# Optimization experiments

Measured on AMD Instinct MI355X. Metric: run time of the kernel, lower is better.

Reference implementation:

```python
import jax, jax.numpy as jnp
import numpy as np

E = 512      # embed_dim
H = 8        # num_heads
HD = E // H  # head_dim
TGT = 512
SRC = 2048
B = 16


def setup_inputs() -> dict:
    key = jax.random.key(0)
    ks = jax.random.split(key, 10)
    inp = {
        "query": jax.random.normal(ks[0], (TGT, B, E), dtype=jnp.float32),
        "key": jax.random.normal(ks[1], (SRC, B, E), dtype=jnp.float32),
        "value": jax.random.normal(ks[2], (SRC, B, E), dtype=jnp.float32),
        "in_proj_weight": jax.random.normal(ks[3], (3 * E, E), dtype=jnp.float32) * 0.02,
        "in_proj_bias": jax.random.normal(ks[4], (3 * E,), dtype=jnp.float32) * 0.02,
        "bias_k": jax.random.normal(ks[5], (1, 1, E), dtype=jnp.float32) * 0.02,
        "bias_v": jax.random.normal(ks[6], (1, 1, E), dtype=jnp.float32) * 0.02,
        "out_proj_weight": jax.random.normal(ks[7], (E, E), dtype=jnp.float32) * 0.02,
        "out_proj_bias": jnp.zeros((E,), dtype=jnp.float32),
        "key_padding_mask": jax.random.randint(ks[8], (B, SRC), 0, 2).astype(bool),
    }
    return inp


def reference(query, key, value, in_proj_weight, in_proj_bias, bias_k, bias_v,
              out_proj_weight, out_proj_bias, key_padding_mask):
    tgt_len, bsz, embed_dim = query.shape
    scaling = float(HD) ** -0.5

    # manual in-projection (query != key, key is value -> separate q, fused kv)
    q = query @ in_proj_weight[:E].T + in_proj_bias[:E]
    k = key @ in_proj_weight[E:2 * E].T + in_proj_bias[E:2 * E]
    v = value @ in_proj_weight[2 * E:].T + in_proj_bias[2 * E:]
    q = q * scaling

    # bias_k / bias_v concatenation along src dim; pad key_padding_mask with False
    k = jnp.concatenate([k, jnp.broadcast_to(bias_k, (1, bsz, E))], axis=0)
    v = jnp.concatenate([v, jnp.broadcast_to(bias_v, (1, bsz, E))], axis=0)
    kpm = jnp.pad(key_padding_mask, ((0, 0), (0, 1)))  # [B, SRC+1]

    src_len = k.shape[0]
    # [len, B, E] -> [B*H, len, HD]
    q = q.reshape(tgt_len, bsz * H, HD).transpose(1, 0, 2)
    k = k.reshape(src_len, bsz * H, HD).transpose(1, 0, 2)
    v = v.reshape(src_len, bsz * H, HD).transpose(1, 0, 2)

    scores = jnp.einsum('bth,bsh->bts', q, k)  # [B*H, TGT, SRC+1]
    mask = kpm[:, None, None, :]               # [B, 1, 1, SRC+1]
    scores = scores.reshape(bsz, H, tgt_len, src_len)
    scores = jnp.where(mask, -jnp.inf, scores).reshape(bsz * H, tgt_len, src_len)
    attn = jax.nn.softmax(scores, axis=-1)

    out = jnp.einsum('bts,bsh->bth', attn, v)                 # [B*H, TGT, HD]
    out = out.transpose(1, 0, 2).reshape(tgt_len, bsz, E)     # [TGT, B, E]
    out = out @ out_proj_weight.T + out_proj_bias
    return out, attn
```

## Files before the change

kernel.cpp:

```cpp
#include <hip/hip_runtime.h>
#include <hip/hip_bf16.h>

#define E    512
#define H    8
#define HD   64
#define TGT  512
#define SRC  2048
#define S1   2049
#define S1P  2112
#define NB   16
#define BH   128
#define NCH  33
#define PW   2120

typedef __attribute__((ext_vector_type(8))) short short8;
typedef __attribute__((ext_vector_type(4))) float floatx4;

__device__ __forceinline__ unsigned short f2bf(float x) {
    unsigned u = __float_as_uint(x);
    u = (u + 0x7FFF + ((u >> 16) & 1)) >> 16;
    return (unsigned short)u;
}

__device__ __forceinline__ int4 cvt8(const float4 f0, const float4 f1) {
    __hip_bfloat162 o[4];
    o[0] = __float22bfloat162_rn({f0.x, f0.y});
    o[1] = __float22bfloat162_rn({f0.z, f0.w});
    o[2] = __float22bfloat162_rn({f1.x, f1.y});
    o[3] = __float22bfloat162_rn({f1.z, f1.w});
    return *(int4*)o;
}

__global__ __launch_bounds__(256) void proj_gemm(const float* __restrict__ X,
    const float* __restrict__ W, const float* __restrict__ bias,
    unsigned short* __restrict__ Y, const int ld, const float scale)
{
    __shared__ __align__(16) unsigned short As[128][72];
    __shared__ __align__(16) unsigned short Bs[64][72];
    const int tid  = threadIdx.x;
    const int c0   = blockIdx.x << 6;
    const int r0   = blockIdx.y << 7;
    const int w    = tid >> 6, lane = tid & 63, c = lane & 15, quad = lane >> 4;
    floatx4 acc[2][4] = {};
    for (int k0 = 0; k0 < E; k0 += 64) {
#pragma unroll
        for (int i = 0; i < 4; ++i) {
            const int idx = tid + (i << 8);
            const int r = idx >> 3, q = (idx & 7) << 3;
            const float4 f0 = *(const float4*)&X[(size_t)(r0 + r) * E + k0 + q];
            const float4 f1 = *(const float4*)&X[(size_t)(r0 + r) * E + k0 + q + 4];
            *(int4*)&As[r][q] = cvt8(f0, f1);
        }
#pragma unroll
        for (int i = 0; i < 2; ++i) {
            const int idx = tid + (i << 8);
            const int r = idx >> 3, q = (idx & 7) << 3;
            const float4 f0 = *(const float4*)&W[(size_t)(c0 + r) * E + k0 + q];
            const float4 f1 = *(const float4*)&W[(size_t)(c0 + r) * E + k0 + q + 4];
            *(int4*)&Bs[r][q] = cvt8(f0, f1);
        }
        __syncthreads();
#pragma unroll
        for (int kh = 0; kh < 2; ++kh) {
            short8 a0 = *(const short8*)&As[(w << 5) + c][(kh << 5) + (quad << 3)];
            short8 a1 = *(const short8*)&As[(w << 5) + 16 + c][(kh << 5) + (quad << 3)];
#pragma unroll
            for (int n = 0; n < 4; ++n) {
                short8 b = *(const short8*)&Bs[(n << 4) + c][(kh << 5) + (quad << 3)];
                acc[0][n] = __builtin_amdgcn_mfma_f32_16x16x32_bf16(a0, b, acc[0][n], 0, 0, 0);
                acc[1][n] = __builtin_amdgcn_mfma_f32_16x16x32_bf16(a1, b, acc[1][n], 0, 0, 0);
            }
        }
        __syncthreads();
    }
#pragma unroll
    for (int mt = 0; mt < 2; ++mt) {
#pragma unroll
        for (int reg = 0; reg < 4; ++reg) {
            const int rg = r0 + (w << 5) + (mt << 4) + (quad << 2) + reg;
            const int t = rg >> 4, b = rg & 15;
#pragma unroll
            for (int n = 0; n < 4; ++n) {
                const int col = c0 + (n << 4) + c;
                const int h = col >> 6, hd = col & 63;
                const float v = (acc[mt][n][reg] + bias[col]) * scale;
                Y[((size_t)(b * H + h) * ld + t) * HD + hd] = f2bf(v);
            }
        }
    }
}

#define FB_BIAS  8192
#define FB_KPAD  64512
#define FB_VPAD  516096
__global__ __launch_bounds__(256) void fill_bias(const float* __restrict__ bk,
    const float* __restrict__ bv,
    unsigned short* __restrict__ kbuf, unsigned short* __restrict__ vtbuf)
{
    const int idx = blockIdx.x * 256 + threadIdx.x;
    if (idx < FB_BIAS) {
        const int bh = idx >> 6, hd = idx & 63, h = bh & 7;
        kbuf[((size_t)bh * S1P + SRC) * HD + hd] = f2bf(bk[h * HD + hd]);
        vtbuf[((size_t)bh * HD + hd) * S1P + SRC] = f2bf(bv[h * HD + hd]);
    } else if (idx < FB_BIAS + FB_KPAD) {
        const int i = idx - FB_BIAS;
        const int bh = i / 504, o = i % 504;
        const int4 z = {0, 0, 0, 0};
        ((int4*)&kbuf[((size_t)bh * S1P + S1) * HD])[o] = z;
    } else if (idx < FB_BIAS + FB_KPAD + FB_VPAD) {
        const int i = idx - FB_BIAS - FB_KPAD;
        const int bh = i / 4032, r = i % 4032;
        const int hd = r / 63, s = S1 + r % 63;
        vtbuf[((size_t)bh * HD + hd) * S1P + s] = 0;
    }
}

__global__ __launch_bounds__(256) void transpose_v(const unsigned short* __restrict__ vbuf,
    unsigned short* __restrict__ vtbuf)
{
    __shared__ __align__(16) unsigned short T[64][72];
    const int tid = threadIdx.x;
    const int s0  = blockIdx.x << 6;
    const int bh  = blockIdx.y;
#pragma unroll
    for (int i = 0; i < 2; ++i) {
        const int idx = tid + (i << 8);
        const int s = idx >> 3, q = (idx & 7) << 3;
        *(int4*)&T[s][q] = *(const int4*)&vbuf[((size_t)bh * SRC + s0 + s) * HD + q];
    }
    __syncthreads();
#pragma unroll
    for (int i = 0; i < 2; ++i) {
        const int idx = tid + (i << 8);
        const int hd = idx >> 3, sq = (idx & 7) << 3;
        unsigned short tmp[8];
#pragma unroll
        for (int j = 0; j < 8; ++j) tmp[j] = T[sq + j][hd];
        *(int4*)&vtbuf[((size_t)bh * HD + hd) * S1P + s0 + sq] = *(int4*)tmp;
    }
}

__global__ __launch_bounds__(512, 4) void attn_fused(
    const unsigned short* __restrict__ qbh,
    const unsigned short* __restrict__ kbuf,
    const unsigned short* __restrict__ vtbuf,
    const int* __restrict__ kpm,
    float* __restrict__ attn, unsigned short* __restrict__ ctx)
{
    __shared__ __align__(16) unsigned short P[16][PW];
    __shared__ float cpart[16][68];
    __shared__ float sums[8][16];
    __shared__ float linv[16];
    const int tid  = threadIdx.x;
    const int orig = blockIdx.y * 32 + blockIdx.x;
    const int swz  = (orig & 7) * 512 + (orig >> 3);
    const int t0   = (swz & 31) << 4;
    const int bh   = swz >> 5;
    const int bb   = bh >> 3;
    const int w = tid >> 6, lane = tid & 63, c = lane & 15, quad = lane >> 4;

    const unsigned short* qr = &qbh[((size_t)bh * TGT + t0 + c) * HD + (quad << 3)];
    short8 qa0 = *(const short8*)qr;
    short8 qa1 = *(const short8*)(qr + 32);

#define LOADK(D0, D1, M, CH) do {                                               \
        const unsigned short* kb_ = &kbuf[((size_t)bh * S1P + ((CH) << 6)) * HD]; \
        _Pragma("unroll")                                                       \
        for (int n_ = 0; n_ < 4; ++n_) {                                        \
            const unsigned short* kr_ = kb_ + ((n_ << 4) + c) * HD + (quad << 3); \
            D0[n_] = *(const short8*)kr_;                                       \
            D1[n_] = *(const short8*)(kr_ + 32);                                \
        }                                                                       \
        _Pragma("unroll")                                                       \
        for (int n_ = 0; n_ < 4; ++n_) {                                        \
            const int s_ = ((CH) << 6) + (n_ << 4) + c;                         \
            M[n_] = (s_ < SRC) ? (kpm[bb * SRC + s_] ? 3e38f : 0.f)             \
                               : ((s_ == SRC) ? 0.f : 3e38f);                   \
        }                                                                       \
    } while (0)

#define QK_COMPUTE(CH, B0, B1, M) do {                                          \
        const int s0_ = (CH) << 6;                                              \
        floatx4 sc_[4] = {};                                                    \
        _Pragma("unroll")                                                       \
        for (int n_ = 0; n_ < 4; ++n_) {                                        \
            sc_[n_] = __builtin_amdgcn_mfma_f32_16x16x32_bf16(qa0, B0[n_], sc_[n_], 0, 0, 0); \
            sc_[n_] = __builtin_amdgcn_mfma_f32_16x16x32_bf16(qa1, B1[n_], sc_[n_], 0, 0, 0); \
        }                                                                       \
        _Pragma("unroll")                                                       \
        for (int n_ = 0; n_ < 4; ++n_) {                                        \
            _Pragma("unroll")                                                   \
            for (int rg_ = 0; rg_ < 4; ++rg_) {                                 \
                const float p_ = __expf(sc_[n_][rg_] - M[n_]);                  \
                rs[rg_] += p_;                                                  \
                P[(quad << 2) + rg_][s0_ + (n_ << 4) + c] = f2bf(p_);           \
            }                                                                   \
        }                                                                       \
    } while (0)

    float rs[4] = {0.f, 0.f, 0.f, 0.f};
    short8 kb0[4], kb1[4];
    float mk[4];
    LOADK(kb0, kb1, mk, w);
    int ch;
    for (ch = w; ch + 8 < NCH; ch += 8) {
        short8 nb0[4], nb1[4];
        float nm[4];
        LOADK(nb0, nb1, nm, ch + 8);
        QK_COMPUTE(ch, kb0, kb1, mk);
#pragma unroll
        for (int n = 0; n < 4; ++n) { kb0[n] = nb0[n]; kb1[n] = nb1[n]; mk[n] = nm[n]; }
    }
    QK_COMPUTE(ch, kb0, kb1, mk);

#pragma unroll
    for (int reg = 0; reg < 4; ++reg) {
        float v = rs[reg];
        v += __shfl_xor(v, 1); v += __shfl_xor(v, 2);
        v += __shfl_xor(v, 4); v += __shfl_xor(v, 8);
        rs[reg] = v;
    }
    if (c == 0) {
#pragma unroll
        for (int reg = 0; reg < 4; ++reg)
            sums[w][(quad << 2) + reg] = rs[reg];
    }
    __syncthreads();
    if (tid < 16) {
        float s = 0.f;
#pragma unroll
        for (int i = 0; i < 8; ++i) s += sums[i][tid];
        linv[tid] = 1.0f / s;
    }
    __syncthreads();

    const int hs = w & 3, kh2 = w >> 2;
    const int base = kh2 * 1056;
    const unsigned short* vrow = &vtbuf[((size_t)bh * HD + (hs << 4) + c) * S1P + base];
#define LV(U) (*(const short8*)&vrow[((U) << 5) + (quad << 3)])
#define LP(U) (*(const short8*)&P[c][base + ((U) << 5) + (quad << 3)])
    floatx4 ca0 = {}, ca1 = {};
    short8 vt = LV(32);
    short8 v0 = LV(0), v1 = LV(1), v2 = LV(2), v3 = LV(3);
#pragma unroll
    for (int u = 0; u < 32; u += 4) {
        ca0 = __builtin_amdgcn_mfma_f32_16x16x32_bf16(LP(u),     v0, ca0, 0, 0, 0);
        ca1 = __builtin_amdgcn_mfma_f32_16x16x32_bf16(LP(u + 1), v1, ca1, 0, 0, 0);
        if (u < 28) { v0 = LV(u + 4); v1 = LV(u + 5); }
        ca0 = __builtin_amdgcn_mfma_f32_16x16x32_bf16(LP(u + 2), v2, ca0, 0, 0, 0);
        ca1 = __builtin_amdgcn_mfma_f32_16x16x32_bf16(LP(u + 3), v3, ca1, 0, 0, 0);
        if (u < 28) { v2 = LV(u + 6); v3 = LV(u + 7); }
    }
    ca0 = __builtin_amdgcn_mfma_f32_16x16x32_bf16(LP(32), vt, ca0, 0, 0, 0);
    if (kh2 == 1) {
#pragma unroll
        for (int reg = 0; reg < 4; ++reg)
            cpart[(quad << 2) + reg][(hs << 4) + c] = ca0[reg] + ca1[reg];
    }
    __syncthreads();
    if (kh2 == 0) {
#pragma unroll
        for (int reg = 0; reg < 4; ++reg) {
            const int row = (quad << 2) + reg;
            const float v = (ca0[reg] + ca1[reg] + cpart[row][(hs << 4) + c]) * linv[row];
            ctx[((size_t)bh * TGT + t0 + row) * HD + (hs << 4) + c] = f2bf(v);
        }
    }

    for (int p = w; p < 16; p += 8) {
        const int s0 = p << 7;
#pragma unroll
        for (int r = 0; r < 16; ++r) {
            const unsigned pk = *(const unsigned*)&P[r][s0 + (lane << 1)];
            const float li = linv[r];
            const size_t a = ((size_t)bh * TGT + t0 + r) * S1 + s0 + (lane << 1);
            attn[a]     = __uint_as_float((pk & 0xFFFFu) << 16) * li;
            attn[a + 1] = __uint_as_float(pk & 0xFFFF0000u) * li;
        }
    }
    if (w == 7 && lane < 16) {
        const float p = __uint_as_float((unsigned)P[lane][2048] << 16) * linv[lane];
        attn[((size_t)bh * TGT + t0 + lane) * S1 + 2048] = p;
    }
#undef LOADK
#undef QK_COMPUTE
#undef LV
#undef LP
}

__global__ __launch_bounds__(256) void outproj_gemm(const unsigned short* __restrict__ ctx,
    const float* __restrict__ W, const float* __restrict__ bias,
    float* __restrict__ out)
{
    __shared__ __align__(16) unsigned short As[128][72];
    __shared__ __align__(16) unsigned short Bs[64][72];
    const int tid = threadIdx.x;
    const int c0  = blockIdx.x << 6;
    const int r0  = blockIdx.y << 7;
    const int w   = tid >> 6, lane = tid & 63, c = lane & 15, quad = lane >> 4;
    floatx4 acc[2][4] = {};
    for (int k0 = 0; k0 < E; k0 += 64) {
        const int h = k0 >> 6;
#pragma unroll
        for (int i = 0; i < 4; ++i) {
            const int idx = tid + (i << 8);
            const int r = idx >> 3, q = (idx & 7) << 3;
            const int rg = r0 + r, t = rg >> 4, b = rg & 15;
            *(int4*)&As[r][q] = *(const int4*)&ctx[((size_t)(b * H + h) * TGT + t) * HD + q];
        }
#pragma unroll
        for (int i = 0; i < 2; ++i) {
            const int idx = tid + (i << 8);
            const int r = idx >> 3, q = (idx & 7) << 3;
            const float4 f0 = *(const float4*)&W[(size_t)(c0 + r) * E + k0 + q];
            const float4 f1 = *(const float4*)&W[(size_t)(c0 + r) * E + k0 + q + 4];
            *(int4*)&Bs[r][q] = cvt8(f0, f1);
        }
        __syncthreads();
#pragma unroll
        for (int kh = 0; kh < 2; ++kh) {
            short8 a0 = *(const short8*)&As[(w << 5) + c][(kh << 5) + (quad << 3)];
            short8 a1 = *(const short8*)&As[(w << 5) + 16 + c][(kh << 5) + (quad << 3)];
#pragma unroll
            for (int n = 0; n < 4; ++n) {
                short8 b = *(const short8*)&Bs[(n << 4) + c][(kh << 5) + (quad << 3)];
                acc[0][n] = __builtin_amdgcn_mfma_f32_16x16x32_bf16(a0, b, acc[0][n], 0, 0, 0);
                acc[1][n] = __builtin_amdgcn_mfma_f32_16x16x32_bf16(a1, b, acc[1][n], 0, 0, 0);
            }
        }
        __syncthreads();
    }
#pragma unroll
    for (int mt = 0; mt < 2; ++mt) {
#pragma unroll
        for (int reg = 0; reg < 4; ++reg) {
            const int rg = r0 + (w << 5) + (mt << 4) + (quad << 2) + reg;
#pragma unroll
            for (int n = 0; n < 4; ++n) {
                const int col = c0 + (n << 4) + c;
                out[(size_t)rg * E + col] = acc[mt][n][reg] + bias[col];
            }
        }
    }
}

extern "C" void kernel_launch(void* const* d_in, const int* in_sizes, int n_in,
                              void* d_out, int out_size, void* d_ws, size_t ws_size,
                              hipStream_t stream)
{
    const float* query  = (const float*)d_in[0];
    const float* key    = (const float*)d_in[1];
    const float* value  = (const float*)d_in[2];
    const float* ipw    = (const float*)d_in[3];
    const float* ipb    = (const float*)d_in[4];
    const float* bias_k = (const float*)d_in[5];
    const float* bias_v = (const float*)d_in[6];
    const float* opw    = (const float*)d_in[7];
    const float* opb    = (const float*)d_in[8];
    const int*   kpm    = (const int*)d_in[9];

    float* out  = (float*)d_out;
    float* attn = out + (size_t)TGT * NB * E;

    unsigned short* vbuf = (unsigned short*)attn;

    char* ws = (char*)d_ws;
    unsigned short* qbh   = (unsigned short*)ws;
    unsigned short* kbuf  = qbh   + (size_t)4194304;
    unsigned short* vtbuf = kbuf  + (size_t)17301504;
    unsigned short* ctx   = vtbuf + (size_t)17301504;

    proj_gemm<<<dim3(8, 64),  256, 0, stream>>>(query, ipw,           ipb,         qbh,  TGT, 0.125f);
    proj_gemm<<<dim3(8, 256), 256, 0, stream>>>(key,   ipw + 262144,  ipb + E,     kbuf, S1P, 1.0f);
    proj_gemm<<<dim3(8, 256), 256, 0, stream>>>(value, ipw + 524288,  ipb + 2 * E, vbuf, SRC, 1.0f);

    fill_bias<<<dim3(2300), 256, 0, stream>>>(bias_k, bias_v, kbuf, vtbuf);
    transpose_v<<<dim3(32, 128), 256, 0, stream>>>(vbuf, vtbuf);

    attn_fused<<<dim3(32, 128), 512, 0, stream>>>(qbh, kbuf, vtbuf, kpm, attn, ctx);
    outproj_gemm<<<dim3(8, 64), 256, 0, stream>>>(ctx, opw, opb, out);
}
```

Measured before the change: 1.123 ms.

## Double attention block to 16 waves and overlap attn store with PV

Raises the attn_fused block from 8 to 16 wavefronts. QK chunks are now striped over 16 waves, and in the PV phase waves 0-7 run the MFMA P·V product at raised priority while waves 8-15 start writing the normalized attention matrix at the same time. It also swaps the manual bf16 rounding for the HIP intrinsic. The aim is to hide the large fp32 attn write behind the PV compute and to add more latency hiding, at the cost of tighter register limits from launch_bounds(1024,8) and fewer blocks resident per CU.

```diff
diff --git a/kernel.cpp b/kernel.cpp
--- a/kernel.cpp
+++ b/kernel.cpp
@@ -20,6 +20,11 @@
     unsigned u = __float_as_uint(x);
     u = (u + 0x7FFF + ((u >> 16) & 1)) >> 16;
     return (unsigned short)u;
+}
+
+__device__ __forceinline__ unsigned short f2bf1(float x) {
+    __hip_bfloat16 h = __float2bfloat16(x);
+    return *(unsigned short*)&h;
 }
 
 __device__ __forceinline__ int4 cvt8(const float4 f0, const float4 f1) {
@@ -140,7 +145,7 @@
     }
 }
 
-__global__ __launch_bounds__(512, 4) void attn_fused(
+__global__ __launch_bounds__(1024, 8) void attn_fused(
     const unsigned short* __restrict__ qbh,
     const unsigned short* __restrict__ kbuf,
     const unsigned short* __restrict__ vtbuf,
@@ -149,7 +154,7 @@
 {
     __shared__ __align__(16) unsigned short P[16][PW];
     __shared__ float cpart[16][68];
-    __shared__ float sums[8][16];
+    __shared__ float sums[16][16];
     __shared__ float linv[16];
     const int tid  = threadIdx.x;
     const int orig = blockIdx.y * 32 + blockIdx.x;
@@ -193,7 +198,7 @@
             for (int rg_ = 0; rg_ < 4; ++rg_) {                                 \
                 const float p_ = __expf(sc_[n_][rg_] - M[n_]);                  \
                 rs[rg_] += p_;                                                  \
-                P[(quad << 2) + rg_][s0_ + (n_ << 4) + c] = f2bf(p_);           \
+                P[(quad << 2) + rg_][s0_ + (n_ << 4) + c] = f2bf1(p_);          \
             }                                                                   \
         }                                                                       \
     } while (0)
@@ -203,10 +208,10 @@
     float mk[4];
     LOADK(kb0, kb1, mk, w);
     int ch;
-    for (ch = w; ch + 8 < NCH; ch += 8) {
+    for (ch = w; ch + 16 < NCH; ch += 16) {
         short8 nb0[4], nb1[4];
         float nm[4];
-        LOADK(nb0, nb1, nm, ch + 8);
+        LOADK(nb0, nb1, nm, ch + 16);
         QK_COMPUTE(ch, kb0, kb1, mk);
 #pragma unroll
         for (int n = 0; n < 4; ++n) { kb0[n] = nb0[n]; kb1[n] = nb1[n]; mk[n] = nm[n]; }
@@ -229,63 +234,77 @@
     if (tid < 16) {
         float s = 0.f;
 #pragma unroll
-        for (int i = 0; i < 8; ++i) s += sums[i][tid];
+        for (int i = 0; i < 16; ++i) s += sums[i][tid];
         linv[tid] = 1.0f / s;
     }
     __syncthreads();
 
-    const int hs = w & 3, kh2 = w >> 2;
-    const int base = kh2 * 1056;
-    const unsigned short* vrow = &vtbuf[((size_t)bh * HD + (hs << 4) + c) * S1P + base];
+#define STORE_PAIR(PP) do {                                                     \
+        const int s0_ = (PP) << 7;                                              \
+        _Pragma("unroll")                                                       \
+        for (int r_ = 0; r_ < 16; ++r_) {                                       \
+            const unsigned pk_ = *(const unsigned*)&P[r_][s0_ + (lane << 1)];   \
+            const float li_ = linv[r_];                                         \
+            const size_t a_ = ((size_t)bh * TGT + t0 + r_) * S1 + s0_ + (lane << 1); \
+            attn[a_]     = __uint_as_float((pk_ & 0xFFFFu) << 16) * li_;        \
+            attn[a_ + 1] = __uint_as_float(pk_ & 0xFFFF0000u) * li_;            \
+        }                                                                       \
+    } while (0)
+
+    const int hs = w & 3, kh2 = (w >> 2) & 1;
+    floatx4 ca0 = {}, ca1 = {};
+    if (w < 8) {
+        const int base = kh2 * 1056;
+        const unsigned short* vrow =
+            &vtbuf[((size_t)bh * HD + (hs << 4) + c) * S1P + base];
 #define LV(U) (*(const short8*)&vrow[((U) << 5) + (quad << 3)])
 #define LP(U) (*(const short8*)&P[c][base + ((U) << 5) + (quad << 3)])
-    floatx4 ca0 = {}, ca1 = {};
-    short8 vt = LV(32);
-    short8 v0 = LV(0), v1 = LV(1), v2 = LV(2), v3 = LV(3);
-#pragma unroll
-    for (int u = 0; u < 32; u += 4) {
-        ca0 = __builtin_amdgcn_mfma_f32_16x16x32_bf16(LP(u),     v0, ca0, 0, 0, 0);
-        ca1 = __builtin_amdgcn_mfma_f32_16x16x32_bf16(LP(u + 1), v1, ca1, 0, 0, 0);
-        if (u < 28) { v0 = LV(u + 4); v1 = LV(u + 5); }
-        ca0 = __builtin_amdgcn_mfma_f32_16x16x32_bf16(LP(u + 2), v2, ca0, 0, 0, 0);
-        ca1 = __builtin_amdgcn_mfma_f32_16x16x32_bf16(LP(u + 3), v3, ca1, 0, 0, 0);
-        if (u < 28) { v2 = LV(u + 6); v3 = LV(u + 7); }
-    }
-    ca0 = __builtin_amdgcn_mfma_f32_16x16x32_bf16(LP(32), vt, ca0, 0, 0, 0);
-    if (kh2 == 1) {
-#pragma unroll
-        for (int reg = 0; reg < 4; ++reg)
-            cpart[(quad << 2) + reg][(hs << 4) + c] = ca0[reg] + ca1[reg];
+        short8 vt = LV(32);
+        short8 v0 = LV(0), v1 = LV(1), v2 = LV(2), v3 = LV(3);
+        __builtin_amdgcn_s_setprio(1);
+#pragma unroll
+        for (int u = 0; u < 32; u += 4) {
+            ca0 = __builtin_amdgcn_mfma_f32_16x16x32_bf16(LP(u),     v0, ca0, 0, 0, 0);
+            ca1 = __builtin_amdgcn_mfma_f32_16x16x32_bf16(LP(u + 1), v1, ca1, 0, 0, 0);
+            if (u < 28) { v0 = LV(u + 4); v1 = LV(u + 5); }
+            ca0 = __builtin_amdgcn_mfma_f32_16x16x32_bf16(LP(u + 2), v2, ca0, 0, 0, 0);
+            ca1 = __builtin_amdgcn_mfma_f32_16x16x32_bf16(LP(u + 3), v3, ca1, 0, 0, 0);
+            if (u < 28) { v2 = LV(u + 6); v3 = LV(u + 7); }
+        }
+        ca0 = __builtin_amdgcn_mfma_f32_16x16x32_bf16(LP(32), vt, ca0, 0, 0, 0);
+        __builtin_amdgcn_s_setprio(0);
+        if (kh2 == 1) {
+#pragma unroll
+            for (int reg = 0; reg < 4; ++reg)
+                cpart[(quad << 2) + reg][(hs << 4) + c] = ca0[reg] + ca1[reg];
+        }
+#undef LV
+#undef LP
+    } else {
+        STORE_PAIR(w - 8);
     }
     __syncthreads();
-    if (kh2 == 0) {
-#pragma unroll
-        for (int reg = 0; reg < 4; ++reg) {
-            const int row = (quad << 2) + reg;
-            const float v = (ca0[reg] + ca1[reg] + cpart[row][(hs << 4) + c]) * linv[row];
-            ctx[((size_t)bh * TGT + t0 + row) * HD + (hs << 4) + c] = f2bf(v);
-        }
-    }
-
-    for (int p = w; p < 16; p += 8) {
-        const int s0 = p << 7;
-#pragma unroll
-        for (int r = 0; r < 16; ++r) {
-            const unsigned pk = *(const unsigned*)&P[r][s0 + (lane << 1)];
-            const float li = linv[r];
-            const size_t a = ((size_t)bh * TGT + t0 + r) * S1 + s0 + (lane << 1);
-            attn[a]     = __uint_as_float((pk & 0xFFFFu) << 16) * li;
-            attn[a + 1] = __uint_as_float(pk & 0xFFFF0000u) * li;
-        }
-    }
-    if (w == 7 && lane < 16) {
-        const float p = __uint_as_float((unsigned)P[lane][2048] << 16) * linv[lane];
-        attn[((size_t)bh * TGT + t0 + lane) * S1 + 2048] = p;
+    if (w < 8) {
+        if (kh2 == 0) {
+#pragma unroll
+            for (int reg = 0; reg < 4; ++reg) {
+                const int row = (quad << 2) + reg;
+                const float v =
+                    (ca0[reg] + ca1[reg] + cpart[row][(hs << 4) + c]) * linv[row];
+                ctx[((size_t)bh * TGT + t0 + row) * HD + (hs << 4) + c] = f2bf1(v);
+            }
+        }
+    } else {
+        STORE_PAIR(w);
+        if (w == 15 && lane < 16) {
+            const float p =
+                __uint_as_float((unsigned)P[lane][2048] << 16) * linv[lane];
+            attn[((size_t)bh * TGT + t0 + lane) * S1 + 2048] = p;
+        }
     }
 #undef LOADK
 #undef QK_COMPUTE
-#undef LV
-#undef LP
+#undef STORE_PAIR
 }
 
 __global__ __launch_bounds__(256) void outproj_gemm(const unsigned short* __restrict__ ctx,
@@ -377,6 +396,6 @@
     fill_bias<<<dim3(2300), 256, 0, stream>>>(bias_k, bias_v, kbuf, vtbuf);
     transpose_v<<<dim3(32, 128), 256, 0, stream>>>(vbuf, vtbuf);
 
-    attn_fused<<<dim3(32, 128), 512, 0, stream>>>(qbh, kbuf, vtbuf, kpm, attn, ctx);
+    attn_fused<<<dim3(32, 128), 1024, 0, stream>>>(qbh, kbuf, vtbuf, kpm, attn, ctx);
     outproj_gemm<<<dim3(8, 64), 256, 0, stream>>>(ctx, opw, opb, out);
 }
```

Measured after the change: 1.119 ms. About the same (-0.3%).
